# Optimization experiments

Hardware: AMD Instinct MI355X
Metric: run time of the kernel (lower is better)

Reference implementation:

```python
import jax, jax.numpy as jnp
import numpy as np

N = 50000
E_RAND = 800000
IN_CH = 128
HID = 64
HEADS = 4
OUT_CH = 3
NEG_SLOPE = 0.2
BN_EPS = 1e-5


def setup_inputs() -> dict:
    key = jax.random.key(0)
    ks = jax.random.split(key, 24)
    x = jax.random.normal(ks[0], (N, IN_CH), dtype=jnp.float32)
    er = jax.random.randint(ks[1], (2, E_RAND), 0, N)
    sl = jnp.tile(jnp.arange(N, dtype=er.dtype)[None, :], (2, 1))
    edge_index = jnp.concatenate([er, sl], axis=1)  # [2, 850000]
    s = 0.1
    d1 = HID * HEADS            # 256
    d2 = (HID // 2) * HEADS     # 128
    inp = dict(x=x, edge_index=edge_index)
    # layer 1: in 128 -> heads*64
    inp["W1"] = s * jax.random.normal(ks[2], (IN_CH, HEADS * HID), dtype=jnp.float32)
    inp["a1s"] = s * jax.random.normal(ks[3], (HEADS, HID), dtype=jnp.float32)
    inp["a1d"] = s * jax.random.normal(ks[4], (HEADS, HID), dtype=jnp.float32)
    inp["b1"] = jnp.zeros((d1,), jnp.float32)
    inp["g1"] = jnp.ones((d1,), jnp.float32)
    inp["be1"] = jnp.zeros((d1,), jnp.float32)
    inp["m1"] = 0.01 * jax.random.normal(ks[5], (d1,), dtype=jnp.float32)
    inp["v1"] = jnp.ones((d1,), jnp.float32) + 0.01 * jax.random.uniform(ks[6], (d1,))
    # layer 2: in 256 -> heads*32
    inp["W2"] = s * jax.random.normal(ks[7], (d1, HEADS * (HID // 2)), dtype=jnp.float32)
    inp["a2s"] = s * jax.random.normal(ks[8], (HEADS, HID // 2), dtype=jnp.float32)
    inp["a2d"] = s * jax.random.normal(ks[9], (HEADS, HID // 2), dtype=jnp.float32)
    inp["b2"] = jnp.zeros((d2,), jnp.float32)
    inp["g2"] = jnp.ones((d2,), jnp.float32)
    inp["be2"] = jnp.zeros((d2,), jnp.float32)
    inp["m2"] = 0.01 * jax.random.normal(ks[10], (d2,), dtype=jnp.float32)
    inp["v2"] = jnp.ones((d2,), jnp.float32) + 0.01 * jax.random.uniform(ks[11], (d2,))
    # layer 3: in 128 -> 1 head, out_ch, concat=False
    inp["W3"] = s * jax.random.normal(ks[12], (d2, OUT_CH), dtype=jnp.float32)
    inp["a3s"] = s * jax.random.normal(ks[13], (1, OUT_CH), dtype=jnp.float32)
    inp["a3d"] = s * jax.random.normal(ks[14], (1, OUT_CH), dtype=jnp.float32)
    inp["b3"] = jnp.zeros((OUT_CH,), jnp.float32)
    return inp


def gat_conv(x, src, dst, W, a_src, a_dst, b, heads, fdim, concat):
    n = x.shape[0]
    h = (x @ W).reshape(n, heads, fdim)           # [N,H,F]
    als = jnp.einsum('nhf,hf->nh', h, a_src)      # [N,H]
    ald = jnp.einsum('nhf,hf->nh', h, a_dst)
    e = jax.nn.leaky_relu(als[src] + ald[dst], NEG_SLOPE)  # [E,H]
    m = jax.lax.stop_gradient(jax.ops.segment_max(e, dst, num_segments=n))
    ex = jnp.exp(e - m[dst])
    ssum = jax.ops.segment_sum(ex, dst, num_segments=n)
    alpha = ex / (ssum[dst] + 1e-16)              # segment softmax over in-edges
    msg = h[src] * alpha[:, :, None]              # [E,H,F]
    out = jax.ops.segment_sum(msg, dst, num_segments=n)  # [N,H,F]
    out = out.reshape(n, heads * fdim) if concat else out.mean(axis=1)
    return out + b


def batch_norm(x, gamma, beta, mean, var):
    return (x - mean) * jax.lax.rsqrt(var + BN_EPS) * gamma + beta


def reference(x, edge_index, W1, a1s, a1d, b1, g1, be1, m1, v1,
              W2, a2s, a2d, b2, g2, be2, m2, v2,
              W3, a3s, a3d, b3):
    src, dst = edge_index[0], edge_index[1]
    h = gat_conv(x, src, dst, W1, a1s, a1d, b1, HEADS, HID, True)
    h = jax.nn.elu(batch_norm(h, g1, be1, m1, v1))
    h = gat_conv(h, src, dst, W2, a2s, a2d, b2, HEADS, HID // 2, True)
    h = jax.nn.elu(batch_norm(h, g2, be2, m2, v2))
    h = gat_conv(h, src, dst, W3, a3s, a3d, b3, 1, OUT_CH, False)
    return jax.nn.log_softmax(h, axis=1)
```

## Files before the change

### kernel.cpp

```cpp
#include <hip/hip_runtime.h>


#define WSZ 64

typedef short short8 __attribute__((ext_vector_type(8)));
typedef short short4v __attribute__((ext_vector_type(4)));
typedef float float4v __attribute__((ext_vector_type(4)));

__device__ inline unsigned short f2bf(float f) {
  unsigned u = __float_as_uint(f);
  u += 0x7FFFu + ((u >> 16) & 1u);
  return (unsigned short)(u >> 16);
}
__device__ inline float bf2f(unsigned short u) {
  return __uint_as_float(((unsigned)u) << 16);
}


__global__ __launch_bounds__(256) void hist_kernel(const int* __restrict__ dst, int E,
                                                   int* __restrict__ deg) {
  int e = blockIdx.x * 256 + threadIdx.x;
  if (e < E) atomicAdd(&deg[dst[e]], 1);
}

__global__ __launch_bounds__(256) void block_sums_kernel(const int* __restrict__ deg, int n,
                                                         int* __restrict__ bsum) {
  __shared__ int sh[256];
  int t = threadIdx.x;
  int base = blockIdx.x * 1024 + t * 4;
  int v = 0;
#pragma unroll
  for (int j = 0; j < 4; ++j) {
    int idx = base + j;
    if (idx < n) v += deg[idx];
  }
  sh[t] = v;
  __syncthreads();
  for (int off = 128; off >= 1; off >>= 1) {
    if (t < off) sh[t] += sh[t + off];
    __syncthreads();
  }
  if (t == 0) bsum[blockIdx.x] = sh[0];
}

__global__ void tiny_scan_kernel(int* bsum, int nb) {
  if (threadIdx.x == 0 && blockIdx.x == 0) {
    int run = 0;
    for (int i = 0; i < nb; ++i) {
      int v = bsum[i];
      bsum[i] = run;
      run += v;
    }
  }
}

__global__ __launch_bounds__(256) void scan_write_kernel(const int* __restrict__ deg, int n,
                                                         const int* __restrict__ bbase,
                                                         int* __restrict__ row_start,
                                                         int* __restrict__ cursor) {
  __shared__ int sh[256];
  int t = threadIdx.x;
  int base = blockIdx.x * 1024 + t * 4;
  int v[4];
  int s = 0;
#pragma unroll
  for (int j = 0; j < 4; ++j) {
    int idx = base + j;
    v[j] = (idx < n) ? deg[idx] : 0;
    s += v[j];
  }
  sh[t] = s;
  __syncthreads();
  for (int off = 1; off < 256; off <<= 1) {
    int x = (t >= off) ? sh[t - off] : 0;
    __syncthreads();
    sh[t] += x;
    __syncthreads();
  }
  int excl = sh[t] - s + bbase[blockIdx.x];
#pragma unroll
  for (int j = 0; j < 4; ++j) {
    int idx = base + j;
    if (idx < n) {
      row_start[idx] = excl;
      cursor[idx] = excl;
    }
    excl += v[j];
  }
  if (blockIdx.x == gridDim.x - 1 && t == 255) row_start[n] = excl;
}

__global__ __launch_bounds__(256) void scatter_kernel(const int* __restrict__ src,
                                                      const int* __restrict__ dst, int E,
                                                      int* __restrict__ cursor,
                                                      int* __restrict__ csr_src) {
  int e = blockIdx.x * 256 + threadIdx.x;
  if (e < E) {
    int d = dst[e];
    int p = atomicAdd(&cursor[d], 1);
    csr_src[p] = src[e];
  }
}


__global__ __launch_bounds__(256) void conv_bf16x4(const float* __restrict__ in,
                                                   unsigned short* __restrict__ out, int n4) {
  int i = blockIdx.x * 256 + threadIdx.x;
  if (i < n4) {
    float4 v = ((const float4*)in)[i];
    ushort4 u;
    u.x = f2bf(v.x); u.y = f2bf(v.y); u.z = f2bf(v.z); u.w = f2bf(v.w);
    ((ushort4*)out)[i] = u;
  }
}

__global__ __launch_bounds__(256) void conv_w1t_kernel(const float* __restrict__ W1,
                                                       unsigned short* __restrict__ W1t) {
  int idx = blockIdx.x * 256 + threadIdx.x;
  int n = idx >> 7, k = idx & 127;
  W1t[idx] = f2bf(W1[k * 256 + n]);
}

__global__ __launch_bounds__(256) void conv_w2t_kernel(const float* __restrict__ W2,
                                                       unsigned short* __restrict__ W2t) {
  int idx = blockIdx.x * 256 + threadIdx.x;
  int n = idx >> 8, p = idx & 255;
  int kl = (p & ~63) | ((p & 3) << 4) | ((p >> 2) & 15);
  W2t[idx] = f2bf(W2[kl * 128 + n]);
}


template <int K, int BN>
__global__ __launch_bounds__(256) void gemm_mfma(
    const unsigned short* __restrict__ A,
    const unsigned short* __restrict__ Bt,
    const float* __restrict__ a_s, const float* __restrict__ a_d,
    unsigned short* __restrict__ hout,
    float* __restrict__ als, float* __restrict__ ald,
    int M) {
  constexpr int CF = BN / 64;
  constexpr int PAD = 36;
  __shared__ unsigned short As[64][PAD];
  __shared__ unsigned short Bs[BN][PAD];
  const int t = threadIdx.x;
  const int w = t >> 6;
  const int lane = t & 63;
  const int c16 = lane & 15;
  const int q = lane >> 4;
  const int bm = blockIdx.x * 64;
  const int arow = t >> 2;
  const int akc = (t & 3) * 8;

  float4v acc[4][CF];
#pragma unroll
  for (int rf = 0; rf < 4; ++rf)
#pragma unroll
    for (int cf = 0; cf < CF; ++cf) acc[rf][cf] = float4v{0.f, 0.f, 0.f, 0.f};

  for (int k0 = 0; k0 < K; k0 += 32) {
    {
      int gr = bm + arow;
      uint4 v = make_uint4(0u, 0u, 0u, 0u);
      if (gr < M) v = *(const uint4*)(A + (size_t)gr * K + k0 + akc);
      *(uint2*)&As[arow][akc] = make_uint2(v.x, v.y);
      *(uint2*)&As[arow][akc + 4] = make_uint2(v.z, v.w);
    }
#pragma unroll
    for (int h = 0; h < BN / 64; ++h) {
      int n = (t >> 2) + h * 64;
      uint4 v = *(const uint4*)(Bt + (size_t)n * K + k0 + akc);
      *(uint2*)&Bs[n][akc] = make_uint2(v.x, v.y);
      *(uint2*)&Bs[n][akc + 4] = make_uint2(v.z, v.w);
    }
    __syncthreads();
    short8 af[4], bfr[CF];
#pragma unroll
    for (int rf = 0; rf < 4; ++rf) {
      short4v lo = *(short4v*)&As[rf * 16 + c16][q * 8];
      short4v hi = *(short4v*)&As[rf * 16 + c16][q * 8 + 4];
      af[rf] = __builtin_shufflevector(lo, hi, 0, 1, 2, 3, 4, 5, 6, 7);
    }
#pragma unroll
    for (int cf = 0; cf < CF; ++cf) {
      int n = w * (CF * 16) + cf * 16 + c16;
      short4v lo = *(short4v*)&Bs[n][q * 8];
      short4v hi = *(short4v*)&Bs[n][q * 8 + 4];
      bfr[cf] = __builtin_shufflevector(lo, hi, 0, 1, 2, 3, 4, 5, 6, 7);
    }
#pragma unroll
    for (int rf = 0; rf < 4; ++rf)
#pragma unroll
      for (int cf = 0; cf < CF; ++cf)
        acc[rf][cf] =
            __builtin_amdgcn_mfma_f32_16x16x32_bf16(af[rf], bfr[cf], acc[rf][cf], 0, 0, 0);
    __syncthreads();
  }

  float sasv[CF], sadv[CF];
#pragma unroll
  for (int cf = 0; cf < CF; ++cf) {
    int L = w * (CF * 16) + cf * 16 + c16;
    sasv[cf] = a_s[L];
    sadv[cf] = a_d[L];
  }
#pragma unroll
  for (int rf = 0; rf < 4; ++rf) {
#pragma unroll
    for (int r = 0; r < 4; ++r) {
      int n = bm + rf * 16 + q * 4 + r;
      float ps = 0.f, pd = 0.f;
      unsigned short us[CF];
#pragma unroll
      for (int cf = 0; cf < CF; ++cf) {
        float v = acc[rf][cf][r];
        us[cf] = f2bf(v);
        ps += v * sasv[cf];
        pd += v * sadv[cf];
      }
#pragma unroll
      for (int off = 1; off <= 8; off <<= 1) {
        ps += __shfl_xor(ps, off, 16);
        pd += __shfl_xor(pd, off, 16);
      }
      if (n < M) {
        if constexpr (CF == 4) {
          ushort4 u;
          u.x = us[0]; u.y = us[1]; u.z = us[2]; u.w = us[3];
          *(ushort4*)(hout + (size_t)n * BN + w * 64 + c16 * 4) = u;
        } else {
          ushort2 u;
          u.x = us[0]; u.y = us[1];
          *(ushort2*)(hout + (size_t)n * BN + w * 32 + c16 * 2) = u;
        }
        if (c16 == 0) {
          als[(size_t)n * 4 + w] = ps;
          ald[(size_t)n * 4 + w] = pd;
        }
      }
    }
  }
}


template <int D, bool OBF>
__global__ __launch_bounds__(256) void gat_aggregate(
    const unsigned short* __restrict__ h_bf, const float* __restrict__ als,
    const float* __restrict__ ald, const int* __restrict__ row_start,
    const int* __restrict__ csr_src, const float* __restrict__ bias,
    const float* __restrict__ gamma, const float* __restrict__ beta,
    const float* __restrict__ bmean, const float* __restrict__ bvar,
    void* __restrict__ outp, int n_nodes) {
  constexpr int VPT = D / WSZ;
  constexpr int H = 4;
  int wid = threadIdx.x >> 6, lane = threadIdx.x & 63;
  int n = blockIdx.x * 4 + wid;
  if (n >= n_nodes) return;
  int c = lane * VPT;
  int hd = lane >> 4;
  float aldv = ald[(size_t)n * H + hd];
  int row = row_start[n], end = row_start[n + 1];
  float acc[VPT] = {};
  float ssum = 0.f;
  int i = row;
  for (; i + 3 < end; i += 4) {
    int s0 = csr_src[i + 0], s1 = csr_src[i + 1];
    int s2 = csr_src[i + 2], s3 = csr_src[i + 3];
    float e0 = als[(size_t)s0 * H + hd] + aldv;
    float e1 = als[(size_t)s1 * H + hd] + aldv;
    float e2 = als[(size_t)s2 * H + hd] + aldv;
    float e3 = als[(size_t)s3 * H + hd] + aldv;
    if constexpr (VPT == 4) {
      ushort4 u0 = *(const ushort4*)(h_bf + (size_t)s0 * D + c);
      ushort4 u1 = *(const ushort4*)(h_bf + (size_t)s1 * D + c);
      ushort4 u2 = *(const ushort4*)(h_bf + (size_t)s2 * D + c);
      ushort4 u3 = *(const ushort4*)(h_bf + (size_t)s3 * D + c);
      e0 = (e0 > 0.f) ? e0 : 0.2f * e0;
      e1 = (e1 > 0.f) ? e1 : 0.2f * e1;
      e2 = (e2 > 0.f) ? e2 : 0.2f * e2;
      e3 = (e3 > 0.f) ? e3 : 0.2f * e3;
      float x0 = __expf(e0), x1 = __expf(e1), x2 = __expf(e2), x3 = __expf(e3);
      ssum += (x0 + x1) + (x2 + x3);
      acc[0] += x0 * bf2f(u0.x) + x1 * bf2f(u1.x) + x2 * bf2f(u2.x) + x3 * bf2f(u3.x);
      acc[1] += x0 * bf2f(u0.y) + x1 * bf2f(u1.y) + x2 * bf2f(u2.y) + x3 * bf2f(u3.y);
      acc[2] += x0 * bf2f(u0.z) + x1 * bf2f(u1.z) + x2 * bf2f(u2.z) + x3 * bf2f(u3.z);
      acc[3] += x0 * bf2f(u0.w) + x1 * bf2f(u1.w) + x2 * bf2f(u2.w) + x3 * bf2f(u3.w);
    } else {
      ushort2 u0 = *(const ushort2*)(h_bf + (size_t)s0 * D + c);
      ushort2 u1 = *(const ushort2*)(h_bf + (size_t)s1 * D + c);
      ushort2 u2 = *(const ushort2*)(h_bf + (size_t)s2 * D + c);
      ushort2 u3 = *(const ushort2*)(h_bf + (size_t)s3 * D + c);
      e0 = (e0 > 0.f) ? e0 : 0.2f * e0;
      e1 = (e1 > 0.f) ? e1 : 0.2f * e1;
      e2 = (e2 > 0.f) ? e2 : 0.2f * e2;
      e3 = (e3 > 0.f) ? e3 : 0.2f * e3;
      float x0 = __expf(e0), x1 = __expf(e1), x2 = __expf(e2), x3 = __expf(e3);
      ssum += (x0 + x1) + (x2 + x3);
      acc[0] += x0 * bf2f(u0.x) + x1 * bf2f(u1.x) + x2 * bf2f(u2.x) + x3 * bf2f(u3.x);
      acc[1] += x0 * bf2f(u0.y) + x1 * bf2f(u1.y) + x2 * bf2f(u2.y) + x3 * bf2f(u3.y);
    }
  }
  for (; i < end; ++i) {
    int s = csr_src[i];
    float e = als[(size_t)s * H + hd] + aldv;
    e = (e > 0.f) ? e : 0.2f * e;
    float ex = __expf(e);
    ssum += ex;
    const unsigned short* hp = h_bf + (size_t)s * D + c;
    if constexpr (VPT == 4) {
      ushort4 u = *(const ushort4*)hp;
      acc[0] += ex * bf2f(u.x);
      acc[1] += ex * bf2f(u.y);
      acc[2] += ex * bf2f(u.z);
      acc[3] += ex * bf2f(u.w);
    } else {
      ushort2 u = *(const ushort2*)hp;
      acc[0] += ex * bf2f(u.x);
      acc[1] += ex * bf2f(u.y);
    }
  }
  float inv = 1.f / (ssum + 1e-16f);
#pragma unroll
  for (int j = 0; j < VPT; ++j) {
    int cl = hd * (VPT * 16) + j * 16 + (lane & 15);
    float o = acc[j] * inv + bias[cl];
    o = (o - bmean[cl]) * rsqrtf(bvar[cl] + 1e-5f) * gamma[cl] + beta[cl];
    o = (o > 0.f) ? o : (__expf(o) - 1.f);
    acc[j] = o;
  }
  if constexpr (OBF) {
    ushort4 u;
    u.x = f2bf(acc[0]); u.y = f2bf(acc[1]); u.z = f2bf(acc[2]); u.w = f2bf(acc[3]);
    *(ushort4*)((unsigned short*)outp + (size_t)n * D + c) = u;
  } else {
    *(float2*)((float*)outp + (size_t)n * D + c) = make_float2(acc[0], acc[1]);
  }
}


__global__ __launch_bounds__(256) void l3_prep_kernel(const float* __restrict__ o2,
                                                      const float* __restrict__ W3,
                                                      const float* __restrict__ a3s,
                                                      const float* __restrict__ a3d,
                                                      float4* __restrict__ h3p,
                                                      float* __restrict__ ald3, int n_nodes) {
  __shared__ float w[384];
  __shared__ float sa[6];
  for (int i = threadIdx.x; i < 384; i += 256) w[i] = W3[i];
  if (threadIdx.x < 3) {
    sa[threadIdx.x] = a3s[threadIdx.x];
    sa[3 + threadIdx.x] = a3d[threadIdx.x];
  }
  __syncthreads();
  int wid = threadIdx.x >> 6, lane = threadIdx.x & 63;
  int n = blockIdx.x * 4 + wid;
  if (n >= n_nodes) return;
  float2 xv = *(const float2*)(o2 + (size_t)n * 128 + lane * 2);
  int k0 = (lane >> 4) * 32 + (lane & 15);
  int k1 = k0 + 16;
  float p0 = xv.x * w[k0 * 3 + 0] + xv.y * w[k1 * 3 + 0];
  float p1 = xv.x * w[k0 * 3 + 1] + xv.y * w[k1 * 3 + 1];
  float p2 = xv.x * w[k0 * 3 + 2] + xv.y * w[k1 * 3 + 2];
#pragma unroll
  for (int off = 32; off >= 1; off >>= 1) {
    p0 += __shfl_xor(p0, off, 64);
    p1 += __shfl_xor(p1, off, 64);
    p2 += __shfl_xor(p2, off, 64);
  }
  if (lane == 0) {
    float als = p0 * sa[0] + p1 * sa[1] + p2 * sa[2];
    float ald = p0 * sa[3] + p1 * sa[4] + p2 * sa[5];
    h3p[n] = make_float4(p0, p1, p2, als);
    ald3[n] = ald;
  }
}


__global__ __launch_bounds__(256) void l3_agg_kernel(const float4* __restrict__ h3p,
                                                     const float* __restrict__ ald3,
                                                     const int* __restrict__ row_start,
                                                     const int* __restrict__ csr_src,
                                                     const float* __restrict__ b3,
                                                     float* __restrict__ out, int n_nodes) {
  int wid = threadIdx.x >> 6, lane = threadIdx.x & 63;
  int n = blockIdx.x * 4 + wid;
  if (n >= n_nodes) return;
  float aldv = ald3[n];
  int row = row_start[n], end = row_start[n + 1];
  float a0 = 0.f, a1 = 0.f, a2 = 0.f, ss = 0.f;
  for (int i = row + lane; i < end; i += 64) {
    int s = csr_src[i];
    float4 hv = h3p[s];
    float e = hv.w + aldv;
    e = (e > 0.f) ? e : 0.2f * e;
    float ex = __expf(e);
    ss += ex;
    a0 += ex * hv.x;
    a1 += ex * hv.y;
    a2 += ex * hv.z;
  }
#pragma unroll
  for (int off = 32; off >= 1; off >>= 1) {
    a0 += __shfl_xor(a0, off, 64);
    a1 += __shfl_xor(a1, off, 64);
    a2 += __shfl_xor(a2, off, 64);
    ss += __shfl_xor(ss, off, 64);
  }
  if (lane == 0) {
    float inv = 1.f / (ss + 1e-16f);
    float o0 = a0 * inv + b3[0];
    float o1 = a1 * inv + b3[1];
    float o2 = a2 * inv + b3[2];
    float m = fmaxf(o0, fmaxf(o1, o2));
    float lse = m + logf(expf(o0 - m) + expf(o1 - m) + expf(o2 - m));
    out[n * 3 + 0] = o0 - lse;
    out[n * 3 + 1] = o1 - lse;
    out[n * 3 + 2] = o2 - lse;
  }
}


extern "C" void kernel_launch(void* const* d_in, const int* in_sizes, int n_in,
                              void* d_out, int out_size, void* d_ws, size_t ws_size,
                              hipStream_t stream) {
  const float* x   = (const float*)d_in[0];
  const int*   ei  = (const int*)d_in[1];
  const float* W1  = (const float*)d_in[2];
  const float* a1s = (const float*)d_in[3];
  const float* a1d = (const float*)d_in[4];
  const float* b1  = (const float*)d_in[5];
  const float* g1v = (const float*)d_in[6];
  const float* be1 = (const float*)d_in[7];
  const float* m1  = (const float*)d_in[8];
  const float* v1  = (const float*)d_in[9];
  const float* W2  = (const float*)d_in[10];
  const float* a2s = (const float*)d_in[11];
  const float* a2d = (const float*)d_in[12];
  const float* b2  = (const float*)d_in[13];
  const float* g2v = (const float*)d_in[14];
  const float* be2 = (const float*)d_in[15];
  const float* m2  = (const float*)d_in[16];
  const float* v2  = (const float*)d_in[17];
  const float* W3  = (const float*)d_in[18];
  const float* a3s = (const float*)d_in[19];
  const float* a3d = (const float*)d_in[20];
  const float* b3  = (const float*)d_in[21];
  float* out = (float*)d_out;

  const int N = in_sizes[0] / 128;
  const int E = in_sizes[1] / 2;
  const int* srcv = ei;
  const int* dstv = ei + E;

  float* wsf  = (float*)d_ws;
  float* o2   = wsf;
  float* als1 = o2 + (size_t)N * 128;
  float* ald1 = als1 + (size_t)N * 4;
  float* als2 = ald1 + (size_t)N * 4;
  float* ald2 = als2 + (size_t)N * 4;
  float* h3p  = ald2 + (size_t)N * 4;
  float* ald3 = h3p + (size_t)N * 4;
  unsigned short* x_bf  = (unsigned short*)(ald3 + N);
  unsigned short* h_bf1 = x_bf + (size_t)N * 128;
  unsigned short* o1_bf = h_bf1 + (size_t)N * 256;
  unsigned short* h_bf2 = o1_bf + (size_t)N * 256;
  unsigned short* W1t   = h_bf2 + (size_t)N * 128;
  unsigned short* W2t   = W1t + 256 * 128;
  int* deg       = (int*)(W2t + 128 * 256);
  int* row_start = deg + N;
  int* cursor    = row_start + (N + 1);
  int* csr_src   = cursor + (N + 1);
  int* bsum      = csr_src + E;

  const int eb = (E + 255) / 256;
  const int nb = (N + 1023) / 1024;
  const int nodes4 = (N + 3) / 4;
  const int mblocks = (N + 63) / 64;

  conv_bf16x4<<<(N * 128 / 4 + 255) / 256, 256, 0, stream>>>(x, x_bf, N * 128 / 4);
  conv_w1t_kernel<<<128, 256, 0, stream>>>(W1, W1t);
  conv_w2t_kernel<<<128, 256, 0, stream>>>(W2, W2t);

  hipMemsetAsync(deg, 0, (size_t)N * sizeof(int), stream);
  hist_kernel<<<eb, 256, 0, stream>>>(dstv, E, deg);
  block_sums_kernel<<<nb, 256, 0, stream>>>(deg, N, bsum);
  tiny_scan_kernel<<<1, 64, 0, stream>>>(bsum, nb);
  scan_write_kernel<<<nb, 256, 0, stream>>>(deg, N, bsum, row_start, cursor);
  scatter_kernel<<<eb, 256, 0, stream>>>(srcv, dstv, E, cursor, csr_src);

  gemm_mfma<128, 256><<<mblocks, 256, 0, stream>>>(x_bf, W1t, a1s, a1d, h_bf1, als1, ald1, N);
  gat_aggregate<256, true><<<nodes4, 256, 0, stream>>>(h_bf1, als1, ald1, row_start, csr_src,
                                                       b1, g1v, be1, m1, v1, o1_bf, N);
  gemm_mfma<256, 128><<<mblocks, 256, 0, stream>>>(o1_bf, W2t, a2s, a2d, h_bf2, als2, ald2, N);
  gat_aggregate<128, false><<<nodes4, 256, 0, stream>>>(h_bf2, als2, ald2, row_start, csr_src,
                                                        b2, g2v, be2, m2, v2, o2, N);
  l3_prep_kernel<<<nodes4, 256, 0, stream>>>(o2, W3, a3s, a3d, (float4*)h3p, ald3, N);
  l3_agg_kernel<<<nodes4, 256, 0, stream>>>((const float4*)h3p, ald3, row_start, csr_src,
                                            b3, out, N);
}
```

Measured before the change: 414.2 us.

## Fuse x bf16 conversion into GEMM and layer-3 prep into aggregation

Removes the separate x-to-bf16 conversion kernel by having the first GEMM load fp32 rows and convert them while staging into shared memory. Folds the layer-3 projection (W3 matvec plus attention logits) into the layer-2 aggregation epilogue, so the fp32 o2 buffer is never written or re-read. Also widens the edge loop to process 8 edges per step before falling back to 4 and 1, giving more gathers in flight. This saves two launches and about 50 MB of global traffic. The cost is a larger fp32 A load in GEMM1 and extra shared memory plus a block barrier in every aggregation block.

```diff
diff --git a/kernel.cpp b/kernel.cpp
--- a/kernel.cpp
+++ b/kernel.cpp
@@ -103,17 +103,6 @@
 }
 
 
-__global__ __launch_bounds__(256) void conv_bf16x4(const float* __restrict__ in,
-                                                   unsigned short* __restrict__ out, int n4) {
-  int i = blockIdx.x * 256 + threadIdx.x;
-  if (i < n4) {
-    float4 v = ((const float4*)in)[i];
-    ushort4 u;
-    u.x = f2bf(v.x); u.y = f2bf(v.y); u.z = f2bf(v.z); u.w = f2bf(v.w);
-    ((ushort4*)out)[i] = u;
-  }
-}
-
 __global__ __launch_bounds__(256) void conv_w1t_kernel(const float* __restrict__ W1,
                                                        unsigned short* __restrict__ W1t) {
   int idx = blockIdx.x * 256 + threadIdx.x;
@@ -130,9 +119,9 @@
 }
 
 
-template <int K, int BN>
+template <int K, int BN, bool AF32>
 __global__ __launch_bounds__(256) void gemm_mfma(
-    const unsigned short* __restrict__ A,
+    const void* __restrict__ Ap,
     const unsigned short* __restrict__ Bt,
     const float* __restrict__ a_s, const float* __restrict__ a_d,
     unsigned short* __restrict__ hout,
@@ -160,10 +149,24 @@
   for (int k0 = 0; k0 < K; k0 += 32) {
     {
       int gr = bm + arow;
-      uint4 v = make_uint4(0u, 0u, 0u, 0u);
-      if (gr < M) v = *(const uint4*)(A + (size_t)gr * K + k0 + akc);
-      *(uint2*)&As[arow][akc] = make_uint2(v.x, v.y);
-      *(uint2*)&As[arow][akc + 4] = make_uint2(v.z, v.w);
+      if constexpr (AF32) {
+        const float* Af = (const float*)Ap + (size_t)gr * K + k0 + akc;
+        float4 v0 = make_float4(0.f, 0.f, 0.f, 0.f), v1 = v0;
+        if (gr < M) {
+          v0 = *(const float4*)Af;
+          v1 = *(const float4*)(Af + 4);
+        }
+        ushort4 u0, u1;
+        u0.x = f2bf(v0.x); u0.y = f2bf(v0.y); u0.z = f2bf(v0.z); u0.w = f2bf(v0.w);
+        u1.x = f2bf(v1.x); u1.y = f2bf(v1.y); u1.z = f2bf(v1.z); u1.w = f2bf(v1.w);
+        *(ushort4*)&As[arow][akc] = u0;
+        *(ushort4*)&As[arow][akc + 4] = u1;
+      } else {
+        uint4 v = make_uint4(0u, 0u, 0u, 0u);
+        if (gr < M) v = *(const uint4*)((const unsigned short*)Ap + (size_t)gr * K + k0 + akc);
+        *(uint2*)&As[arow][akc] = make_uint2(v.x, v.y);
+        *(uint2*)&As[arow][akc + 4] = make_uint2(v.z, v.w);
+      }
     }
 #pragma unroll
     for (int h = 0; h < BN / 64; ++h) {
@@ -242,16 +245,30 @@
 }
 
 
-template <int D, bool OBF>
+template <int D, bool FUSEL3>
 __global__ __launch_bounds__(256) void gat_aggregate(
     const unsigned short* __restrict__ h_bf, const float* __restrict__ als,
     const float* __restrict__ ald, const int* __restrict__ row_start,
     const int* __restrict__ csr_src, const float* __restrict__ bias,
     const float* __restrict__ gamma, const float* __restrict__ beta,
     const float* __restrict__ bmean, const float* __restrict__ bvar,
-    void* __restrict__ outp, int n_nodes) {
+    unsigned short* __restrict__ obf,
+    const float* __restrict__ W3, const float* __restrict__ a3s,
+    const float* __restrict__ a3d, float4* __restrict__ h3p,
+    float* __restrict__ ald3,
+    int n_nodes) {
   constexpr int VPT = D / WSZ;
   constexpr int H = 4;
+  __shared__ float w3s[384];
+  __shared__ float sa3[6];
+  if constexpr (FUSEL3) {
+    for (int i = threadIdx.x; i < 384; i += 256) w3s[i] = W3[i];
+    if (threadIdx.x < 3) {
+      sa3[threadIdx.x] = a3s[threadIdx.x];
+      sa3[3 + threadIdx.x] = a3d[threadIdx.x];
+    }
+    __syncthreads();
+  }
   int wid = threadIdx.x >> 6, lane = threadIdx.x & 63;
   int n = blockIdx.x * 4 + wid;
   if (n >= n_nodes) return;
@@ -262,62 +279,48 @@
   float acc[VPT] = {};
   float ssum = 0.f;
   int i = row;
-  for (; i + 3 < end; i += 4) {
-    int s0 = csr_src[i + 0], s1 = csr_src[i + 1];
-    int s2 = csr_src[i + 2], s3 = csr_src[i + 3];
-    float e0 = als[(size_t)s0 * H + hd] + aldv;
-    float e1 = als[(size_t)s1 * H + hd] + aldv;
-    float e2 = als[(size_t)s2 * H + hd] + aldv;
-    float e3 = als[(size_t)s3 * H + hd] + aldv;
-    if constexpr (VPT == 4) {
-      ushort4 u0 = *(const ushort4*)(h_bf + (size_t)s0 * D + c);
-      ushort4 u1 = *(const ushort4*)(h_bf + (size_t)s1 * D + c);
-      ushort4 u2 = *(const ushort4*)(h_bf + (size_t)s2 * D + c);
-      ushort4 u3 = *(const ushort4*)(h_bf + (size_t)s3 * D + c);
-      e0 = (e0 > 0.f) ? e0 : 0.2f * e0;
-      e1 = (e1 > 0.f) ? e1 : 0.2f * e1;
-      e2 = (e2 > 0.f) ? e2 : 0.2f * e2;
-      e3 = (e3 > 0.f) ? e3 : 0.2f * e3;
-      float x0 = __expf(e0), x1 = __expf(e1), x2 = __expf(e2), x3 = __expf(e3);
-      ssum += (x0 + x1) + (x2 + x3);
-      acc[0] += x0 * bf2f(u0.x) + x1 * bf2f(u1.x) + x2 * bf2f(u2.x) + x3 * bf2f(u3.x);
-      acc[1] += x0 * bf2f(u0.y) + x1 * bf2f(u1.y) + x2 * bf2f(u2.y) + x3 * bf2f(u3.y);
-      acc[2] += x0 * bf2f(u0.z) + x1 * bf2f(u1.z) + x2 * bf2f(u2.z) + x3 * bf2f(u3.z);
-      acc[3] += x0 * bf2f(u0.w) + x1 * bf2f(u1.w) + x2 * bf2f(u2.w) + x3 * bf2f(u3.w);
-    } else {
-      ushort2 u0 = *(const ushort2*)(h_bf + (size_t)s0 * D + c);
-      ushort2 u1 = *(const ushort2*)(h_bf + (size_t)s1 * D + c);
-      ushort2 u2 = *(const ushort2*)(h_bf + (size_t)s2 * D + c);
-      ushort2 u3 = *(const ushort2*)(h_bf + (size_t)s3 * D + c);
-      e0 = (e0 > 0.f) ? e0 : 0.2f * e0;
-      e1 = (e1 > 0.f) ? e1 : 0.2f * e1;
-      e2 = (e2 > 0.f) ? e2 : 0.2f * e2;
-      e3 = (e3 > 0.f) ? e3 : 0.2f * e3;
-      float x0 = __expf(e0), x1 = __expf(e1), x2 = __expf(e2), x3 = __expf(e3);
-      ssum += (x0 + x1) + (x2 + x3);
-      acc[0] += x0 * bf2f(u0.x) + x1 * bf2f(u1.x) + x2 * bf2f(u2.x) + x3 * bf2f(u3.x);
-      acc[1] += x0 * bf2f(u0.y) + x1 * bf2f(u1.y) + x2 * bf2f(u2.y) + x3 * bf2f(u3.y);
-    }
-  }
-  for (; i < end; ++i) {
-    int s = csr_src[i];
-    float e = als[(size_t)s * H + hd] + aldv;
-    e = (e > 0.f) ? e : 0.2f * e;
-    float ex = __expf(e);
-    ssum += ex;
-    const unsigned short* hp = h_bf + (size_t)s * D + c;
-    if constexpr (VPT == 4) {
-      ushort4 u = *(const ushort4*)hp;
-      acc[0] += ex * bf2f(u.x);
-      acc[1] += ex * bf2f(u.y);
-      acc[2] += ex * bf2f(u.z);
-      acc[3] += ex * bf2f(u.w);
-    } else {
-      ushort2 u = *(const ushort2*)hp;
-      acc[0] += ex * bf2f(u.x);
-      acc[1] += ex * bf2f(u.y);
-    }
-  }
+
+#define EDGE_BLOCK(B)                                                          \
+  for (; i + (B) - 1 < end; i += (B)) {                                        \
+    int s[B];                                                                  \
+    float e[B];                                                                \
+    _Pragma("unroll") for (int j = 0; j < (B); ++j) s[j] = csr_src[i + j];     \
+    _Pragma("unroll") for (int j = 0; j < (B); ++j) e[j] =                     \
+        als[(size_t)s[j] * H + hd] + aldv;                                     \
+    if constexpr (VPT == 4) {                                                  \
+      ushort4 u[B];                                                            \
+      _Pragma("unroll") for (int j = 0; j < (B); ++j) u[j] =                   \
+          *(const ushort4*)(h_bf + (size_t)s[j] * D + c);                      \
+      _Pragma("unroll") for (int j = 0; j < (B); ++j) {                        \
+        float ee = e[j];                                                       \
+        ee = (ee > 0.f) ? ee : 0.2f * ee;                                      \
+        float ex = __expf(ee);                                                 \
+        ssum += ex;                                                            \
+        acc[0] += ex * bf2f(u[j].x);                                           \
+        acc[1] += ex * bf2f(u[j].y);                                           \
+        acc[2] += ex * bf2f(u[j].z);                                           \
+        acc[3] += ex * bf2f(u[j].w);                                           \
+      }                                                                        \
+    } else {                                                                   \
+      ushort2 u[B];                                                            \
+      _Pragma("unroll") for (int j = 0; j < (B); ++j) u[j] =                   \
+          *(const ushort2*)(h_bf + (size_t)s[j] * D + c);                      \
+      _Pragma("unroll") for (int j = 0; j < (B); ++j) {                        \
+        float ee = e[j];                                                       \
+        ee = (ee > 0.f) ? ee : 0.2f * ee;                                      \
+        float ex = __expf(ee);                                                 \
+        ssum += ex;                                                            \
+        acc[0] += ex * bf2f(u[j].x);                                           \
+        acc[1] += ex * bf2f(u[j].y);                                           \
+      }                                                                        \
+    }                                                                          \
+  }
+
+  EDGE_BLOCK(8)
+  EDGE_BLOCK(4)
+  EDGE_BLOCK(1)
+#undef EDGE_BLOCK
+
   float inv = 1.f / (ssum + 1e-16f);
 #pragma unroll
   for (int j = 0; j < VPT; ++j) {
@@ -327,50 +330,28 @@
     o = (o > 0.f) ? o : (__expf(o) - 1.f);
     acc[j] = o;
   }
-  if constexpr (OBF) {
+  if constexpr (!FUSEL3) {
     ushort4 u;
     u.x = f2bf(acc[0]); u.y = f2bf(acc[1]); u.z = f2bf(acc[2]); u.w = f2bf(acc[3]);
-    *(ushort4*)((unsigned short*)outp + (size_t)n * D + c) = u;
+    *(ushort4*)(obf + (size_t)n * D + c) = u;
   } else {
-    *(float2*)((float*)outp + (size_t)n * D + c) = make_float2(acc[0], acc[1]);
-  }
-}
-
-
-__global__ __launch_bounds__(256) void l3_prep_kernel(const float* __restrict__ o2,
-                                                      const float* __restrict__ W3,
-                                                      const float* __restrict__ a3s,
-                                                      const float* __restrict__ a3d,
-                                                      float4* __restrict__ h3p,
-                                                      float* __restrict__ ald3, int n_nodes) {
-  __shared__ float w[384];
-  __shared__ float sa[6];
-  for (int i = threadIdx.x; i < 384; i += 256) w[i] = W3[i];
-  if (threadIdx.x < 3) {
-    sa[threadIdx.x] = a3s[threadIdx.x];
-    sa[3 + threadIdx.x] = a3d[threadIdx.x];
-  }
-  __syncthreads();
-  int wid = threadIdx.x >> 6, lane = threadIdx.x & 63;
-  int n = blockIdx.x * 4 + wid;
-  if (n >= n_nodes) return;
-  float2 xv = *(const float2*)(o2 + (size_t)n * 128 + lane * 2);
-  int k0 = (lane >> 4) * 32 + (lane & 15);
-  int k1 = k0 + 16;
-  float p0 = xv.x * w[k0 * 3 + 0] + xv.y * w[k1 * 3 + 0];
-  float p1 = xv.x * w[k0 * 3 + 1] + xv.y * w[k1 * 3 + 1];
-  float p2 = xv.x * w[k0 * 3 + 2] + xv.y * w[k1 * 3 + 2];
-#pragma unroll
-  for (int off = 32; off >= 1; off >>= 1) {
-    p0 += __shfl_xor(p0, off, 64);
-    p1 += __shfl_xor(p1, off, 64);
-    p2 += __shfl_xor(p2, off, 64);
-  }
-  if (lane == 0) {
-    float als = p0 * sa[0] + p1 * sa[1] + p2 * sa[2];
-    float ald = p0 * sa[3] + p1 * sa[4] + p2 * sa[5];
-    h3p[n] = make_float4(p0, p1, p2, als);
-    ald3[n] = ald;
+    int k0l = hd * 32 + (lane & 15);
+    int k1l = k0l + 16;
+    float p0 = acc[0] * w3s[k0l * 3 + 0] + acc[1] * w3s[k1l * 3 + 0];
+    float p1 = acc[0] * w3s[k0l * 3 + 1] + acc[1] * w3s[k1l * 3 + 1];
+    float p2 = acc[0] * w3s[k0l * 3 + 2] + acc[1] * w3s[k1l * 3 + 2];
+#pragma unroll
+    for (int off = 32; off >= 1; off >>= 1) {
+      p0 += __shfl_xor(p0, off, 64);
+      p1 += __shfl_xor(p1, off, 64);
+      p2 += __shfl_xor(p2, off, 64);
+    }
+    if (lane == 0) {
+      float als3 = p0 * sa3[0] + p1 * sa3[1] + p2 * sa3[2];
+      float ad3 = p0 * sa3[3] + p1 * sa3[4] + p2 * sa3[5];
+      h3p[n] = make_float4(p0, p1, p2, als3);
+      ald3[n] = ad3;
+    }
   }
 }
 
@@ -452,15 +433,13 @@
   const int* dstv = ei + E;
 
   float* wsf  = (float*)d_ws;
-  float* o2   = wsf;
-  float* als1 = o2 + (size_t)N * 128;
+  float* als1 = wsf;
   float* ald1 = als1 + (size_t)N * 4;
   float* als2 = ald1 + (size_t)N * 4;
   float* ald2 = als2 + (size_t)N * 4;
   float* h3p  = ald2 + (size_t)N * 4;
   float* ald3 = h3p + (size_t)N * 4;
-  unsigned short* x_bf  = (unsigned short*)(ald3 + N);
-  unsigned short* h_bf1 = x_bf + (size_t)N * 128;
+  unsigned short* h_bf1 = (unsigned short*)(ald3 + N);
   unsigned short* o1_bf = h_bf1 + (size_t)N * 256;
   unsigned short* h_bf2 = o1_bf + (size_t)N * 256;
   unsigned short* W1t   = h_bf2 + (size_t)N * 128;
@@ -476,7 +455,6 @@
   const int nodes4 = (N + 3) / 4;
   const int mblocks = (N + 63) / 64;
 
-  conv_bf16x4<<<(N * 128 / 4 + 255) / 256, 256, 0, stream>>>(x, x_bf, N * 128 / 4);
   conv_w1t_kernel<<<128, 256, 0, stream>>>(W1, W1t);
   conv_w2t_kernel<<<128, 256, 0, stream>>>(W2, W2t);
 
@@ -487,13 +465,16 @@
   scan_write_kernel<<<nb, 256, 0, stream>>>(deg, N, bsum, row_start, cursor);
   scatter_kernel<<<eb, 256, 0, stream>>>(srcv, dstv, E, cursor, csr_src);
 
-  gemm_mfma<128, 256><<<mblocks, 256, 0, stream>>>(x_bf, W1t, a1s, a1d, h_bf1, als1, ald1, N);
-  gat_aggregate<256, true><<<nodes4, 256, 0, stream>>>(h_bf1, als1, ald1, row_start, csr_src,
-                                                       b1, g1v, be1, m1, v1, o1_bf, N);
-  gemm_mfma<256, 128><<<mblocks, 256, 0, stream>>>(o1_bf, W2t, a2s, a2d, h_bf2, als2, ald2, N);
-  gat_aggregate<128, false><<<nodes4, 256, 0, stream>>>(h_bf2, als2, ald2, row_start, csr_src,
-                                                        b2, g2v, be2, m2, v2, o2, N);
-  l3_prep_kernel<<<nodes4, 256, 0, stream>>>(o2, W3, a3s, a3d, (float4*)h3p, ald3, N);
+  gemm_mfma<128, 256, true><<<mblocks, 256, 0, stream>>>(x, W1t, a1s, a1d, h_bf1, als1,
+                                                         ald1, N);
+  gat_aggregate<256, false><<<nodes4, 256, 0, stream>>>(
+      h_bf1, als1, ald1, row_start, csr_src, b1, g1v, be1, m1, v1, o1_bf, nullptr, nullptr,
+      nullptr, nullptr, nullptr, N);
+  gemm_mfma<256, 128, false><<<mblocks, 256, 0, stream>>>(o1_bf, W2t, a2s, a2d, h_bf2, als2,
+                                                          ald2, N);
+  gat_aggregate<128, true><<<nodes4, 256, 0, stream>>>(
+      h_bf2, als2, ald2, row_start, csr_src, b2, g2v, be2, m2, v2, nullptr, W3, a3s, a3d,
+      (float4*)h3p, ald3, N);
   l3_agg_kernel<<<nodes4, 256, 0, stream>>>((const float4*)h3p, ald3, row_start, csr_src,
                                             b3, out, N);
 }
```

Result: faster. 382.4 us (-7.7%).
